# Optimization experiments

Measured on AMD Instinct MI355X. Metric: run time of the kernel, lower is better.

The kernel has to match this reference:

```python
import jax, jax.numpy as jnp
import numpy as np

N = 10000      # nodes
E = 160000     # edges
C = 128        # channels (hidden_irreps multiplicity)
NE = 10        # num_elements
G = 16         # num graphs
NB = 8         # num_bessel
RMAX = 5.0
PCUT = 5.0     # num_polynomial_cutoff
AVG_NN = 16.0
SQ3 = 3.0 ** 0.5


def _mlp(x, w1, w2, w3, wo):
    h = jax.nn.silu(x @ w1)
    h = jax.nn.silu(h @ w2)
    h = jax.nn.silu(h @ w3)
    return h @ wo


def _forward(positions, node_attrs, charges, shifts,
             W_emb, W_up1, Wr1_1, Wr1_2, Wr1_3, Wr1_o, Wlin1_s, Wlin1_v,
             P1_s1, P1_ss, P1_vv, P1_v1, P1_sv, Lp1_s, Lp1_v, R1,
             Wsk, Wup2_s, Wup2_v, Wr2_1, Wr2_2, Wr2_3, Wr2_o, Wlin2_s, Wlin2_v,
             P2_v1, P2_sv, Lp2_v, Rmid, Rout,
             edge_index, batch, num_graphs):
    snd, rcv = edge_index[0], edge_index[1]
    # edge vectors / lengths
    vec = positions[rcv] - positions[snd] + shifts                  # [E,3]
    length = jnp.sqrt(jnp.sum(vec * vec, -1) + 1e-12)               # [E]
    Yv = SQ3 * vec / length[:, None]                                # l=1 SH, component norm
    # Bessel radial basis * polynomial cutoff
    n = jnp.arange(1, NB + 1, dtype=positions.dtype)
    bess = (2.0 / RMAX) ** 0.5 * jnp.sin(n * jnp.pi * length[:, None] / RMAX) / length[:, None]
    u = length / RMAX
    p = PCUT
    fcut = jnp.where(u < 1.0,
                     1 - ((p + 1) * (p + 2) / 2) * u ** p + p * (p + 2) * u ** (p + 1)
                     - (p * (p + 1) / 2) * u ** (p + 2), 0.0)
    edge_feats = bess * fcut[:, None]                               # [E,NB]

    h = node_attrs @ W_emb                                          # node embedding [N,C]
    seg = lambda m: jax.ops.segment_sum(m, rcv, num_segments=N) / AVG_NN
    we = lambda Pm: node_attrs @ Pm                                 # element-dep. weights

    # ---- interaction / product / readout layer 1 (node feats are scalars) ----
    hu = h @ W_up1
    w = _mlp(edge_feats, Wr1_1, Wr1_2, Wr1_3, Wr1_o)                # [E,2C] TP weights
    w_ss, w_sv = w[:, :C], w[:, C:]
    hs_e = hu[snd]                                                  # gather sender feats
    A_s = seg(w_ss * hs_e)                                          # 0e x 0e -> 0e
    A_v = seg((w_sv * hs_e)[:, :, None] * Yv[:, None, :])           # 0e x 1o -> 1o
    A_s = A_s @ Wlin1_s
    A_v = jnp.einsum('ncd,ce->ned', A_v, Wlin1_v)
    # symmetric contraction (correlation=2), element-dependent weights
    B_s = we(P1_s1) * A_s + we(P1_ss) * A_s * A_s + we(P1_vv) * jnp.sum(A_v * A_v, -1) / SQ3
    B_v = we(P1_v1)[:, :, None] * A_v + we(P1_sv)[:, :, None] * A_s[:, :, None] * A_v
    h_s = B_s @ Lp1_s
    h_v = jnp.einsum('ncd,ce->ned', B_v, Lp1_v)
    dip1 = jnp.einsum('ncd,c->nd', h_v, R1)                         # linear dipole readout

    # ---- layer 2 (residual, output 128x1o) ----
    hs = h_s @ Wup2_s
    hv = jnp.einsum('ncd,ce->ned', h_v, Wup2_v)
    w2 = _mlp(edge_feats, Wr2_1, Wr2_2, Wr2_3, Wr2_o)               # [E,4C]
    w_a, w_b, w_c, w_d = w2[:, :C], w2[:, C:2 * C], w2[:, 2 * C:3 * C], w2[:, 3 * C:]
    hs_e, hv_e = hs[snd], hv[snd]
    m_s = w_a * hs_e + w_b * jnp.einsum('ecd,ed->ec', hv_e, Yv) / SQ3   # 0x0, 1x1->0
    m_v = (w_c * hs_e)[:, :, None] * Yv[:, None, :] + w_d[:, :, None] * hv_e  # 0x1,1x0->1
    A2_s = seg(m_s) @ Wlin2_s
    A2_v = jnp.einsum('ncd,ce->ned', seg(m_v), Wlin2_v)
    sc_v = jnp.einsum('ne,ecf,ncd->nfd', node_attrs, Wsk, h_v)      # skip TP (residual)
    B2_v = we(P2_v1)[:, :, None] * A2_v + we(P2_sv)[:, :, None] * A2_s[:, :, None] * A2_v
    h2_v = jnp.einsum('ncd,ce->ned', B2_v, Lp2_v) + sc_v
    # nonlinear dipole readout: input is pure 1o so gate scalars have no equivariant
    # path (zeros) -> sigmoid(0)=0.5 multiplier, as e3nn Gate would compute.
    mid = 0.5 * jnp.einsum('ncd,ck->nkd', h2_v, Rmid)               # [N,16,3]
    dip2 = jnp.einsum('nkd,k->nd', mid, Rout)

    atomic_dipoles = dip1 + dip2                                    # [N,3]
    total = jax.ops.segment_sum(atomic_dipoles, batch, num_segments=num_graphs)
    baseline = jax.ops.segment_sum(charges[:, None] * positions, batch, num_segments=num_graphs)
    return total + baseline, atomic_dipoles


def setup_inputs() -> dict:
    key = jax.random.key(0)
    ks = jax.random.split(key, 40)
    f32 = jnp.float32
    species = jax.random.randint(ks[0], (N,), 0, NE)
    w = lambda k, shape: jax.random.normal(k, shape, f32) / np.sqrt(shape[-2] if len(shape) > 1 else shape[0]).astype(np.float32)
    inp = dict(
        positions=jax.random.uniform(ks[1], (N, 3), f32) * 6.0,
        node_attrs=jax.nn.one_hot(species, NE, dtype=f32),
        charges=jax.random.normal(ks[2], (N,), f32),
        shifts=jnp.zeros((E, 3), f32),
        edge_index=jax.random.randint(ks[3], (2, E), 0, N),
        batch=jnp.sort(jax.random.randint(ks[4], (N,), 0, G)),
        ptr=jnp.arange(G + 1),
        W_emb=w(ks[5], (NE, C)), W_up1=w(ks[6], (C, C)),
        Wr1_1=w(ks[7], (NB, 64)), Wr1_2=w(ks[8], (64, 64)), Wr1_3=w(ks[9], (64, 64)),
        Wr1_o=w(ks[10], (64, 2 * C)), Wlin1_s=w(ks[11], (C, C)), Wlin1_v=w(ks[12], (C, C)),
        P1_s1=w(ks[13], (NE, C)), P1_ss=w(ks[14], (NE, C)), P1_vv=w(ks[15], (NE, C)),
        P1_v1=w(ks[16], (NE, C)), P1_sv=w(ks[17], (NE, C)),
        Lp1_s=w(ks[18], (C, C)), Lp1_v=w(ks[19], (C, C)),
        R1=jax.random.normal(ks[20], (C,), f32) / np.float32(np.sqrt(C)),
        Wsk=jax.random.normal(ks[21], (NE, C, C), f32) / np.float32(np.sqrt(C)),
        Wup2_s=w(ks[22], (C, C)), Wup2_v=w(ks[23], (C, C)),
        Wr2_1=w(ks[24], (NB, 64)), Wr2_2=w(ks[25], (64, 64)), Wr2_3=w(ks[26], (64, 64)),
        Wr2_o=w(ks[27], (64, 4 * C)), Wlin2_s=w(ks[28], (C, C)), Wlin2_v=w(ks[29], (C, C)),
        P2_v1=w(ks[30], (NE, C)), P2_sv=w(ks[31], (NE, C)), Lp2_v=w(ks[32], (C, C)),
        Rmid=w(ks[33], (C, 16)),
        Rout=jax.random.normal(ks[34], (16,), f32) / 4.0,
    )
    return inp


def reference(positions, node_attrs, charges, shifts, edge_index, batch, ptr,
              W_emb, W_up1, Wr1_1, Wr1_2, Wr1_3, Wr1_o, Wlin1_s, Wlin1_v,
              P1_s1, P1_ss, P1_vv, P1_v1, P1_sv, Lp1_s, Lp1_v, R1,
              Wsk, Wup2_s, Wup2_v, Wr2_1, Wr2_2, Wr2_3, Wr2_o, Wlin2_s, Wlin2_v,
              P2_v1, P2_sv, Lp2_v, Rmid, Rout):
    num_graphs = ptr.shape[0] - 1
    return _forward(positions, node_attrs, charges, shifts,
                    W_emb, W_up1, Wr1_1, Wr1_2, Wr1_3, Wr1_o, Wlin1_s, Wlin1_v,
                    P1_s1, P1_ss, P1_vv, P1_v1, P1_sv, Lp1_s, Lp1_v, R1,
                    Wsk, Wup2_s, Wup2_v, Wr2_1, Wr2_2, Wr2_3, Wr2_o, Wlin2_s, Wlin2_v,
                    P2_v1, P2_sv, Lp2_v, Rmid, Rout,
                    edge_index, batch, num_graphs)
```

## Files before the change

kernel.cpp:

```cpp
#include <hip/hip_runtime.h>

#define NN 10000
#define EE 160000
#define CC 128
#define NEL 10
#define NGR 16

static inline int cdiv(int a, int b) { return (a + b - 1) / b; }

__device__ __forceinline__ float silu_f(float x) { return x / (1.0f + __expf(-x)); }

__device__ __forceinline__ float bf2f(unsigned short u) {
    unsigned int x = ((unsigned int)u) << 16;
    return __uint_as_float(x);
}
__device__ __forceinline__ unsigned short f2bf(float f) {
    unsigned int x = __float_as_uint(f);
    unsigned int r = x + 0x7fffu + ((x >> 16) & 1u);
    return (unsigned short)(r >> 16);
}

typedef __attribute__((ext_vector_type(8))) short bf16x8;
typedef __attribute__((ext_vector_type(4))) float f32x4;

template <int K, int N, int MODE>
__global__ __launch_bounds__(256) void mfma_gemm(
    const unsigned short* __restrict__ in, int in_ld,
    const unsigned short* __restrict__ Wt,
    unsigned short* __restrict__ out, int out_ld,
    int R)
{
    constexpr int NT = N / 16;
    constexpr int KC = K / 32;
    constexpr int CPR = K / 8;
    __shared__ __align__(16) unsigned short Ash[64 * K];
    __shared__ __align__(16) unsigned short Bsh[N * K];

    const int tid = threadIdx.x;
    const int w = tid >> 6;
    const int l = tid & 63;
    const int row0 = blockIdx.x * 64;
    const int cb = blockIdx.y * N;

    for (int cid = tid; cid < 64 * CPR; cid += 256) {
        int r = cid / CPR, k8 = cid % CPR;
        int row = row0 + r;
        uint4 val = make_uint4(0u, 0u, 0u, 0u);
        if (row < R) val = *(const uint4*)(in + (size_t)row * in_ld + k8 * 8);
        unsigned bo = ((unsigned)(r * K + k8 * 8) * 2u) ^ (((unsigned)(r & 7)) << 4);
        *(uint4*)((char*)Ash + bo) = val;
    }
    for (int cid = tid; cid < N * CPR; cid += 256) {
        int nn = cid / CPR, k8 = cid % CPR;
        uint4 val = *(const uint4*)(Wt + (size_t)(cb + nn) * K + k8 * 8);
        unsigned bo = ((unsigned)(nn * K + k8 * 8) * 2u) ^ (((unsigned)(nn & 7)) << 4);
        *(uint4*)((char*)Bsh + bo) = val;
    }
    __syncthreads();

    bf16x8 afr[KC];
#pragma unroll
    for (int kc = 0; kc < KC; ++kc) {
        int r = w * 16 + (l & 15);
        int k = kc * 32 + (l >> 4) * 8;
        unsigned bo = ((unsigned)(r * K + k) * 2u) ^ (((unsigned)(r & 7)) << 4);
        afr[kc] = *(const bf16x8*)((char*)Ash + bo);
    }

    f32x4 acc[NT];
#pragma unroll
    for (int nt = 0; nt < NT; ++nt) {
        acc[nt] = (f32x4){0.f, 0.f, 0.f, 0.f};
#pragma unroll
        for (int kc = 0; kc < KC; ++kc) {
            int col = nt * 16 + (l & 15);
            int k = kc * 32 + (l >> 4) * 8;
            unsigned bo = ((unsigned)(col * K + k) * 2u) ^ (((unsigned)(col & 7)) << 4);
            bf16x8 bfr = *(const bf16x8*)((char*)Bsh + bo);
            acc[nt] = __builtin_amdgcn_mfma_f32_16x16x32_bf16(afr[kc], bfr, acc[nt], 0, 0, 0);
        }
    }

#pragma unroll
    for (int nt = 0; nt < NT; ++nt) {
#pragma unroll
        for (int rg = 0; rg < 4; ++rg) {
            int row = row0 + w * 16 + (l >> 4) * 4 + rg;
            if (row < R) {
                int col = cb + nt * 16 + (l & 15);
                float v = acc[nt][rg];
                if constexpr (MODE == 1) v = silu_f(v);
                out[(size_t)row * out_ld + col] = f2bf(v);
            }
        }
    }
}

template <int K, int N, int MODE>
__global__ __launch_bounds__(256) void mfma_gemm_f32(
    const float* __restrict__ in, int in_ld,
    const unsigned short* __restrict__ Wt,
    float* __restrict__ out, int out_ld,
    int R, float scale)
{
    constexpr int NT = N / 16;
    constexpr int KC = K / 32;
    constexpr int CPR = K / 8;
    __shared__ __align__(16) unsigned short Ash[64 * K];
    __shared__ __align__(16) unsigned short Bsh[N * K];

    const int tid = threadIdx.x;
    const int w = tid >> 6;
    const int l = tid & 63;
    const int row0 = blockIdx.x * 64;
    const int cb = blockIdx.y * N;

    for (int cid = tid; cid < 64 * CPR; cid += 256) {
        int r = cid / CPR, k8 = cid % CPR;
        int row = row0 + r;
        union { unsigned short u16[8]; uint4 v; } pk;
        if (row < R) {
            const float* p = in + (size_t)row * in_ld + k8 * 8;
            float4 f0 = *(const float4*)p;
            float4 f1 = *(const float4*)(p + 4);
            pk.u16[0] = f2bf(f0.x); pk.u16[1] = f2bf(f0.y);
            pk.u16[2] = f2bf(f0.z); pk.u16[3] = f2bf(f0.w);
            pk.u16[4] = f2bf(f1.x); pk.u16[5] = f2bf(f1.y);
            pk.u16[6] = f2bf(f1.z); pk.u16[7] = f2bf(f1.w);
        } else {
            pk.v = make_uint4(0u, 0u, 0u, 0u);
        }
        unsigned bo = ((unsigned)(r * K + k8 * 8) * 2u) ^ (((unsigned)(r & 7)) << 4);
        *(uint4*)((char*)Ash + bo) = pk.v;
    }
    for (int cid = tid; cid < N * CPR; cid += 256) {
        int nn = cid / CPR, k8 = cid % CPR;
        uint4 val = *(const uint4*)(Wt + (size_t)(cb + nn) * K + k8 * 8);
        unsigned bo = ((unsigned)(nn * K + k8 * 8) * 2u) ^ (((unsigned)(nn & 7)) << 4);
        *(uint4*)((char*)Bsh + bo) = val;
    }
    __syncthreads();

    bf16x8 afr[KC];
#pragma unroll
    for (int kc = 0; kc < KC; ++kc) {
        int r = w * 16 + (l & 15);
        int k = kc * 32 + (l >> 4) * 8;
        unsigned bo = ((unsigned)(r * K + k) * 2u) ^ (((unsigned)(r & 7)) << 4);
        afr[kc] = *(const bf16x8*)((char*)Ash + bo);
    }

    f32x4 acc[NT];
#pragma unroll
    for (int nt = 0; nt < NT; ++nt) {
        acc[nt] = (f32x4){0.f, 0.f, 0.f, 0.f};
#pragma unroll
        for (int kc = 0; kc < KC; ++kc) {
            int col = nt * 16 + (l & 15);
            int k = kc * 32 + (l >> 4) * 8;
            unsigned bo = ((unsigned)(col * K + k) * 2u) ^ (((unsigned)(col & 7)) << 4);
            bf16x8 bfr = *(const bf16x8*)((char*)Bsh + bo);
            acc[nt] = __builtin_amdgcn_mfma_f32_16x16x32_bf16(afr[kc], bfr, acc[nt], 0, 0, 0);
        }
    }

#pragma unroll
    for (int nt = 0; nt < NT; ++nt) {
#pragma unroll
        for (int rg = 0; rg < 4; ++rg) {
            int row = row0 + w * 16 + (l >> 4) * 4 + rg;
            if (row < R) {
                int col = cb + nt * 16 + (l & 15);
                float v = acc[nt][rg] * scale;
                size_t idx = (size_t)row * out_ld + col;
                if constexpr (MODE == 6)      out[idx] += v;
                else if constexpr (MODE == 2) ((unsigned short*)out)[idx] = f2bf(v);
                else                          out[idx] = v;
            }
        }
    }
}

struct WPE { const float* s[8]; unsigned short* d[8]; int K[8], N[8], Kp[8]; };
__global__ void k_wprepE(WPE wp)
{
    int m = blockIdx.y;
    int i = blockIdx.x * 256 + threadIdx.x;
    int tot = wp.N[m] * wp.Kp[m];
    if (i >= tot) return;
    int n = i / wp.Kp[m], k = i % wp.Kp[m];
    wp.d[m][i] = (k < wp.K[m]) ? f2bf(wp.s[m][k * wp.N[m] + n]) : (unsigned short)0;
}

struct WP10 { const float* s[10]; unsigned short* d[10]; };
__global__ void k_wprep10(WP10 wp)
{
    int m = blockIdx.y;
    int i = blockIdx.x * 256 + threadIdx.x;
    if (i >= 128 * 128) return;
    int n = i / 128, k = i % 128;
    wp.d[m][i] = f2bf(wp.s[m][k * 128 + n]);
}

__global__ void k_count(const int* __restrict__ rcv, int* __restrict__ deg)
{
    int e = blockIdx.x * 256 + threadIdx.x;
    if (e < EE) atomicAdd(&deg[rcv[e]], 1);
}

__global__ __launch_bounds__(256) void k_scan(const int* __restrict__ deg,
                                              int* __restrict__ rowptr,
                                              int* __restrict__ cursor)
{
    __shared__ int part[256];
    const int t = threadIdx.x;
    const int PER = (NN + 255) / 256;
    int base = t * PER;
    int s = 0;
    for (int j = 0; j < PER; ++j) { int idx = base + j; if (idx < NN) s += deg[idx]; }
    part[t] = s;
    __syncthreads();
    for (int off = 1; off < 256; off <<= 1) {
        int v = (t >= off) ? part[t - off] : 0;
        __syncthreads();
        part[t] += v;
        __syncthreads();
    }
    int run = (t == 0) ? 0 : part[t - 1];
    for (int j = 0; j < PER; ++j) {
        int idx = base + j;
        if (idx < NN) { rowptr[idx] = run; cursor[idx] = run; run += deg[idx]; }
    }
    if (t == 255) rowptr[NN] = part[255];
}

__global__ void k_fill(const int* __restrict__ rcv, int* __restrict__ cursor,
                       int* __restrict__ perm)
{
    int e = blockIdx.x * 256 + threadIdx.x;
    if (e >= EE) return;
    int pos = atomicAdd(&cursor[rcv[e]], 1);
    perm[pos] = e;
}

__global__ __launch_bounds__(256) void k_sortwave(const int* __restrict__ rowptr,
                                                  int* __restrict__ perm)
{
    int gid = blockIdx.x * 256 + threadIdx.x;
    int wid = gid >> 6;
    int lane = gid & 63;
    if (wid >= NN) return;
    int a = rowptr[wid], b = rowptr[wid + 1];
    int d = b - a;
    if (d <= 1) return;
    if (d <= 64) {
        int v = (lane < d) ? perm[a + lane] : 0x7fffffff;
        int rank = 0;
        for (int j = 0; j < 64; ++j) {
            int vj = __shfl(v, j);
            if (j < d && vj < v) ++rank;
        }
        if (lane < d) perm[a + rank] = v;
    } else if (lane == 0) {
        for (int i = a + 1; i < b; ++i) {
            int v = perm[i]; int j = i - 1;
            while (j >= a && perm[j] > v) { perm[j + 1] = perm[j]; --j; }
            perm[j + 1] = v;
        }
    }
}

__global__ void k_geom_perm(const float* __restrict__ pos, const float* __restrict__ shifts,
                            const int* __restrict__ snd, const int* __restrict__ rcv,
                            const int* __restrict__ perm,
                            float* __restrict__ Yv, unsigned short* __restrict__ efb,
                            int* __restrict__ psnd)
{
    int i = blockIdx.x * 256 + threadIdx.x;
    if (i >= EE) return;
    int e = perm[i];
    int s = snd[e], r = rcv[e];
    psnd[i] = s;
    float vx = pos[r * 3 + 0] - pos[s * 3 + 0] + shifts[e * 3 + 0];
    float vy = pos[r * 3 + 1] - pos[s * 3 + 1] + shifts[e * 3 + 1];
    float vz = pos[r * 3 + 2] - pos[s * 3 + 2] + shifts[e * 3 + 2];
    float len = sqrtf(vx * vx + vy * vy + vz * vz + 1e-12f);
    float inv = 1.0f / len;
    const float SQ3 = 1.7320508075688772f;
    Yv[i * 3 + 0] = SQ3 * vx * inv;
    Yv[i * 3 + 1] = SQ3 * vy * inv;
    Yv[i * 3 + 2] = SQ3 * vz * inv;
    float u = len * 0.2f;
    float fc = 0.0f;
    if (u < 1.0f) {
        float u2 = u * u, u4 = u2 * u2, u5 = u4 * u, u6 = u5 * u, u7 = u6 * u;
        fc = 1.0f - 21.0f * u5 + 35.0f * u6 - 15.0f * u7;
    }
    float pref = 0.6324555320336759f * inv * fc;
    const float PIO5 = 0.6283185307179586f;
    union { unsigned short u16[8]; uint4 v; } pk;
#pragma unroll
    for (int n = 1; n <= 8; ++n)
        pk.u16[n - 1] = f2bf(pref * sinf((float)n * PIO5 * len));
    uint4* dst = (uint4*)(efb + (size_t)i * 32);
    dst[0] = pk.v;
    dst[1] = make_uint4(0u, 0u, 0u, 0u);
    dst[2] = make_uint4(0u, 0u, 0u, 0u);
    dst[3] = make_uint4(0u, 0u, 0u, 0u);
}

__global__ __launch_bounds__(256) void k_gather1(
    const int* __restrict__ rowptr, const int* __restrict__ psnd,
    const float* __restrict__ Yv, const unsigned short* __restrict__ wb,
    int e0, int e1,
    const unsigned short* __restrict__ gS,
    float* __restrict__ outS, float* __restrict__ outV)
{
    const int t = threadIdx.x;
    const int c = t & 127;
    const int n = blockIdx.x * 2 + (t >> 7);
    if (n >= NN) return;
    int rs = rowptr[n], re = rowptr[n + 1];
    if (rs < e0) rs = e0;
    if (re > e1) re = e1;
    if (rs >= re) return;
    float accs = 0.f, a0 = 0.f, a1 = 0.f, a2 = 0.f;
    for (int i = rs; i < re; ++i) {
        const unsigned short* wp = wb + (size_t)(i - e0) * 256;
        float wss = bf2f(wp[c]);
        float wsv = bf2f(wp[128 + c]);
        float h = bf2f(gS[psnd[i] * 128 + c]);
        float y0 = Yv[i * 3], y1 = Yv[i * 3 + 1], y2 = Yv[i * 3 + 2];
        accs = fmaf(wss, h, accs);
        float tv = wsv * h;
        a0 = fmaf(tv, y0, a0); a1 = fmaf(tv, y1, a1); a2 = fmaf(tv, y2, a2);
    }
    outS[n * 128 + c] += accs;
    outV[n * 384 + c]       += a0;
    outV[n * 384 + 128 + c] += a1;
    outV[n * 384 + 256 + c] += a2;
}

__global__ __launch_bounds__(256) void k_gather23(
    const int* __restrict__ rowptr, const int* __restrict__ psnd,
    const float* __restrict__ Yv, const unsigned short* __restrict__ wb,
    int e0, int e1,
    const unsigned short* __restrict__ gS, const unsigned short* __restrict__ gV,
    float* __restrict__ outS, float* __restrict__ outV)
{
    const int t = threadIdx.x;
    const int c = t & 127;
    const int n = blockIdx.x * 2 + (t >> 7);
    if (n >= NN) return;
    int rs = rowptr[n], re = rowptr[n + 1];
    if (rs < e0) rs = e0;
    if (re > e1) re = e1;
    if (rs >= re) return;
    float accs = 0.f, a0 = 0.f, a1 = 0.f, a2 = 0.f;
    for (int i = rs; i < re; ++i) {
        const unsigned short* wp = wb + (size_t)(i - e0) * 512;
        float wa = bf2f(wp[c]);
        float wbv = bf2f(wp[128 + c]);
        float wc = bf2f(wp[256 + c]);
        float wd = bf2f(wp[384 + c]);
        int s = psnd[i];
        float hs = bf2f(gS[s * 128 + c]);
        float v0 = bf2f(gV[s * 384 + c]);
        float v1 = bf2f(gV[s * 384 + 128 + c]);
        float v2 = bf2f(gV[s * 384 + 256 + c]);
        float y0 = Yv[i * 3], y1 = Yv[i * 3 + 1], y2 = Yv[i * 3 + 2];
        float hd = v0 * y0 + v1 * y1 + v2 * y2;
        accs = fmaf(wa, hs, accs);
        accs = fmaf(wbv, hd * 0.57735026919f, accs);
        float tv = wc * hs;
        a0 = fmaf(tv, y0, a0); a0 = fmaf(wd, v0, a0);
        a1 = fmaf(tv, y1, a1); a1 = fmaf(wd, v1, a1);
        a2 = fmaf(tv, y2, a2); a2 = fmaf(wd, v2, a2);
    }
    outS[n * 128 + c] += accs;
    outV[n * 384 + c]       += a0;
    outV[n * 384 + 128 + c] += a1;
    outV[n * 384 + 256 + c] += a2;
}

__global__ void k_species(const float* __restrict__ attrs, int* __restrict__ species)
{
    int n = blockIdx.x * 256 + threadIdx.x;
    if (n >= NN) return;
    int sp = 0;
#pragma unroll
    for (int j = 0; j < NEL; ++j)
        if (attrs[n * NEL + j] > 0.5f) sp = j;
    species[n] = sp;
}

__global__ void k_embed(const float* __restrict__ W_emb, const int* __restrict__ species,
                        float* __restrict__ h)
{
    int t = blockIdx.x * 256 + threadIdx.x;
    if (t >= NN * CC) return;
    int n = t >> 7, c = t & 127;
    h[t] = W_emb[species[n] * CC + c];
}

__global__ void k_rmix(const float* __restrict__ Rmid, const float* __restrict__ Rout,
                       float* __restrict__ rmix)
{
    int c = threadIdx.x;
    float s = 0.f;
#pragma unroll
    for (int k = 0; k < 16; ++k) s = fmaf(Rmid[c * 16 + k], Rout[k], s);
    rmix[c] = s;
}

__global__ void k_B1(const int* __restrict__ species,
                     const float* __restrict__ As_l, const float* __restrict__ Av_l,
                     const float* __restrict__ P_s1, const float* __restrict__ P_ss,
                     const float* __restrict__ P_vv, const float* __restrict__ P_v1,
                     const float* __restrict__ P_sv,
                     float* __restrict__ Bs, float* __restrict__ Bv)
{
    int t = blockIdx.x * 256 + threadIdx.x;
    if (t >= NN * CC) return;
    int n = t >> 7, c = t & 127;
    int sp = species[n];
    int pb = sp * CC + c;
    int vb = n * 384 + c;
    float as = As_l[t];
    float a0 = Av_l[vb], a1 = Av_l[vb + CC], a2 = Av_l[vb + 2 * CC];
    Bs[t] = P_s1[pb] * as + P_ss[pb] * as * as
          + P_vv[pb] * (a0 * a0 + a1 * a1 + a2 * a2) * 0.57735026919f;
    float tv = P_v1[pb] + P_sv[pb] * as;
    Bv[vb] = tv * a0; Bv[vb + CC] = tv * a1; Bv[vb + 2 * CC] = tv * a2;
}

__global__ void k_B2(const int* __restrict__ species,
                     const float* __restrict__ As_l, const float* __restrict__ Av_l,
                     const float* __restrict__ P_v1, const float* __restrict__ P_sv,
                     float* __restrict__ Bv)
{
    int t = blockIdx.x * 256 + threadIdx.x;
    if (t >= NN * CC) return;
    int n = t >> 7, c = t & 127;
    int sp = species[n];
    int pb = sp * CC + c;
    int vb = n * 384 + c;
    float as = As_l[t];
    float tv = P_v1[pb] + P_sv[pb] * as;
    Bv[vb] = tv * Av_l[vb];
    Bv[vb + CC] = tv * Av_l[vb + CC];
    Bv[vb + 2 * CC] = tv * Av_l[vb + 2 * CC];
}

__global__ void k_dip1(const float* __restrict__ h_v, const float* __restrict__ R1,
                       float* __restrict__ dip1)
{
    int n = blockIdx.x, l = threadIdx.x;
    const float* hb = h_v + n * 384;
#pragma unroll
    for (int d = 0; d < 3; ++d) {
        float v = hb[d * CC + l] * R1[l] + hb[d * CC + 64 + l] * R1[64 + l];
        for (int o = 32; o > 0; o >>= 1) v += __shfl_down(v, o);
        if (l == 0) dip1[n * 3 + d] = v;
    }
}

__global__ void k_sc(const int* __restrict__ species, const float* __restrict__ h_v,
                     const float* __restrict__ Wsk, float* __restrict__ h2v)
{
    int n = blockIdx.x, f = threadIdx.x;
    int sp = species[n];
    const float* Wp = Wsk + sp * (CC * CC);
    const float* hvn = h_v + n * 384;
    float a0 = 0.f, a1 = 0.f, a2 = 0.f;
    for (int c = 0; c < CC; ++c) {
        float w = Wp[c * CC + f];
        a0 = fmaf(hvn[c], w, a0);
        a1 = fmaf(hvn[CC + c], w, a1);
        a2 = fmaf(hvn[2 * CC + c], w, a2);
    }
    h2v[n * 384 + f] = a0;
    h2v[n * 384 + CC + f] = a1;
    h2v[n * 384 + 2 * CC + f] = a2;
}

__global__ void k_node_out(const float* __restrict__ h2v, const float* __restrict__ rmix,
                           const float* __restrict__ dip1,
                           const float* __restrict__ charges, const float* __restrict__ pos,
                           float* __restrict__ out, float* __restrict__ tot)
{
    int n = blockIdx.x, l = threadIdx.x;
    const float* hb = h2v + n * 384;
    float r0 = rmix[l], r1 = rmix[64 + l];
    float red[3];
#pragma unroll
    for (int d = 0; d < 3; ++d) {
        float v = hb[d * CC + l] * r0 + hb[d * CC + 64 + l] * r1;
        for (int o = 32; o > 0; o >>= 1) v += __shfl_down(v, o);
        red[d] = v;
    }
    if (l == 0) {
        float q = charges[n];
#pragma unroll
        for (int d = 0; d < 3; ++d) {
            float a = dip1[n * 3 + d] + 0.5f * red[d];
            out[48 + n * 3 + d] = a;
            tot[n * 3 + d] = a + q * pos[n * 3 + d];
        }
    }
}

__global__ __launch_bounds__(256) void k_greduce(const float* __restrict__ tot,
                                                 const int* __restrict__ batch,
                                                 float* __restrict__ out)
{
    __shared__ float r[256 * 3];
    const int g = blockIdx.x;
    const int t = threadIdx.x;
    float s0 = 0.f, s1 = 0.f, s2 = 0.f;
    for (int n = t; n < NN; n += 256) {
        if (batch[n] == g) {
            s0 += tot[n * 3]; s1 += tot[n * 3 + 1]; s2 += tot[n * 3 + 2];
        }
    }
    r[t] = s0; r[256 + t] = s1; r[512 + t] = s2;
    __syncthreads();
    for (int off = 128; off > 0; off >>= 1) {
        if (t < off) {
            r[t] += r[t + off];
            r[256 + t] += r[256 + t + off];
            r[512 + t] += r[512 + t + off];
        }
        __syncthreads();
    }
    if (t < 3) out[g * 3 + t] = r[t * 256];
}

extern "C" void kernel_launch(void* const* d_in, const int* in_sizes, int n_in,
                              void* d_out, int out_size, void* d_ws, size_t ws_size,
                              hipStream_t stream)
{
    const float* positions = (const float*)d_in[0];
    const float* node_attrs = (const float*)d_in[1];
    const float* charges = (const float*)d_in[2];
    const float* shifts = (const float*)d_in[3];
    const int*   eidx = (const int*)d_in[4];
    const int*   batch = (const int*)d_in[5];
    const float* W_emb  = (const float*)d_in[7];
    const float* W_up1  = (const float*)d_in[8];
    const float* Wr1_1  = (const float*)d_in[9];
    const float* Wr1_2  = (const float*)d_in[10];
    const float* Wr1_3  = (const float*)d_in[11];
    const float* Wr1_o  = (const float*)d_in[12];
    const float* Wlin1_s = (const float*)d_in[13];
    const float* Wlin1_v = (const float*)d_in[14];
    const float* P1_s1 = (const float*)d_in[15];
    const float* P1_ss = (const float*)d_in[16];
    const float* P1_vv = (const float*)d_in[17];
    const float* P1_v1 = (const float*)d_in[18];
    const float* P1_sv = (const float*)d_in[19];
    const float* Lp1_s = (const float*)d_in[20];
    const float* Lp1_v = (const float*)d_in[21];
    const float* R1    = (const float*)d_in[22];
    const float* Wsk   = (const float*)d_in[23];
    const float* Wup2_s = (const float*)d_in[24];
    const float* Wup2_v = (const float*)d_in[25];
    const float* Wr2_1 = (const float*)d_in[26];
    const float* Wr2_2 = (const float*)d_in[27];
    const float* Wr2_3 = (const float*)d_in[28];
    const float* Wr2_o = (const float*)d_in[29];
    const float* Wlin2_s = (const float*)d_in[30];
    const float* Wlin2_v = (const float*)d_in[31];
    const float* P2_v1 = (const float*)d_in[32];
    const float* P2_sv = (const float*)d_in[33];
    const float* Lp2_v = (const float*)d_in[34];
    const float* Rmid  = (const float*)d_in[35];
    const float* Rout  = (const float*)d_in[36];
    (void)in_sizes; (void)n_in; (void)out_size;

    const int* snd = eidx;
    const int* rcv = eidx + EE;
    float* out = (float*)d_out;

    char* ws = (char*)d_ws;
    size_t off = 0;
    auto alloc = [&](size_t bytes) -> void* {
        void* p = (void*)(ws + off);
        off = (off + bytes + 255) & ~(size_t)255;
        return p;
    };
    int*   species = (int*)alloc((size_t)NN * 4);
    int*   deg     = (int*)alloc((size_t)NN * 4);
    int*   rowptr  = (int*)alloc((size_t)(NN + 16) * 4);
    int*   cursor  = (int*)alloc((size_t)NN * 4);
    int*   perm    = (int*)alloc((size_t)EE * 4);
    int*   psnd    = (int*)alloc((size_t)EE * 4);
    float* Yv   = (float*)alloc((size_t)EE * 3 * 4);
    unsigned short* efb = (unsigned short*)alloc((size_t)EE * 32 * 2);
    float* A_s  = (float*)alloc((size_t)NN * CC * 4);
    float* A_v  = (float*)alloc((size_t)NN * 3 * CC * 4);
    float* hbuf = (float*)alloc((size_t)NN * CC * 4);
    float* hu   = (float*)alloc((size_t)NN * CC * 4);
    float* h_v  = (float*)alloc((size_t)NN * 3 * CC * 4);
    float* h2v  = (float*)alloc((size_t)NN * 3 * CC * 4);
    float* dip1 = (float*)alloc((size_t)NN * 3 * 4);
    float* rmix = (float*)alloc((size_t)CC * 4);
    float* tot  = (float*)alloc((size_t)NN * 3 * 4);
    unsigned short* hub = (unsigned short*)alloc((size_t)NN * CC * 2);
    unsigned short* hsb = (unsigned short*)alloc((size_t)NN * CC * 2);
    unsigned short* hvb = (unsigned short*)alloc((size_t)NN * 3 * CC * 2);
    unsigned short* W1t_l1 = (unsigned short*)alloc(64 * 32 * 2);
    unsigned short* W2t_l1 = (unsigned short*)alloc(64 * 64 * 2);
    unsigned short* W3t_l1 = (unsigned short*)alloc(64 * 64 * 2);
    unsigned short* Wot_l1 = (unsigned short*)alloc(256 * 64 * 2);
    unsigned short* W1t_l2 = (unsigned short*)alloc(64 * 32 * 2);
    unsigned short* W2t_l2 = (unsigned short*)alloc(64 * 64 * 2);
    unsigned short* W3t_l2 = (unsigned short*)alloc(64 * 64 * 2);
    unsigned short* Wot_l2 = (unsigned short*)alloc(512 * 64 * 2);
    unsigned short* Wn[10];
    for (int m = 0; m < 10; ++m) Wn[m] = (unsigned short*)alloc(128 * 128 * 2);
    unsigned short* hbA = (unsigned short*)alloc((size_t)EE * 64 * 2);
    unsigned short* hbB = (unsigned short*)alloc((size_t)EE * 64 * 2);

    int C = 16;
    if      (off + (size_t)EE * 512 * 2 + 4096 <= ws_size)        C = 1;
    else if (off + (size_t)(EE / 2) * 512 * 2 + 4096 <= ws_size)  C = 2;
    else if (off + (size_t)(EE / 4) * 512 * 2 + 4096 <= ws_size)  C = 4;
    else if (off + (size_t)(EE / 8) * 512 * 2 + 4096 <= ws_size)  C = 8;
    const int EC = EE / C;
    unsigned short* wbuf = (unsigned short*)alloc((size_t)EC * 512 * 2);

    const float inv16 = 1.0f / 16.0f;
    const float one = 1.0f;

    hipMemsetAsync(deg, 0, (size_t)NN * 4, stream);
    hipMemsetAsync(A_s, 0, (size_t)NN * CC * 4, stream);
    hipMemsetAsync(A_v, 0, (size_t)NN * 3 * CC * 4, stream);

    {
        WPE wp;
        const float* s[8] = {Wr1_1, Wr1_2, Wr1_3, Wr1_o, Wr2_1, Wr2_2, Wr2_3, Wr2_o};
        unsigned short* d[8] = {W1t_l1, W2t_l1, W3t_l1, Wot_l1, W1t_l2, W2t_l2, W3t_l2, Wot_l2};
        int Ks[8] = {8, 64, 64, 64, 8, 64, 64, 64};
        int Ns[8] = {64, 64, 64, 256, 64, 64, 64, 512};
        int Kp[8] = {32, 64, 64, 64, 32, 64, 64, 64};
        for (int m = 0; m < 8; ++m) { wp.s[m] = s[m]; wp.d[m] = d[m]; wp.K[m] = Ks[m]; wp.N[m] = Ns[m]; wp.Kp[m] = Kp[m]; }
        k_wprepE<<<dim3(cdiv(512 * 64, 256), 8), 256, 0, stream>>>(wp);
    }
    {
        WP10 wp;
        const float* srcs[10] = {W_up1, Wlin1_s, Wlin1_v, Lp1_s, Lp1_v,
                                 Wup2_s, Wup2_v, Wlin2_s, Wlin2_v, Lp2_v};
        for (int m = 0; m < 10; ++m) { wp.s[m] = srcs[m]; wp.d[m] = Wn[m]; }
        k_wprep10<<<dim3(cdiv(128 * 128, 256), 10), 256, 0, stream>>>(wp);
    }

    k_count<<<cdiv(EE, 256), 256, 0, stream>>>(rcv, deg);
    k_scan<<<1, 256, 0, stream>>>(deg, rowptr, cursor);
    k_fill<<<cdiv(EE, 256), 256, 0, stream>>>(rcv, cursor, perm);
    k_sortwave<<<cdiv(NN * 64, 256), 256, 0, stream>>>(rowptr, perm);
    k_geom_perm<<<cdiv(EE, 256), 256, 0, stream>>>(positions, shifts, snd, rcv, perm, Yv, efb, psnd);

    k_species<<<cdiv(NN, 256), 256, 0, stream>>>(node_attrs, species);
    k_embed<<<cdiv(NN * CC, 256), 256, 0, stream>>>(W_emb, species, hbuf);
    k_rmix<<<1, CC, 0, stream>>>(Rmid, Rout, rmix);

    mfma_gemm_f32<128, 128, 2><<<cdiv(NN, 64), 256, 0, stream>>>(
        hbuf, 128, Wn[0], (float*)hub, 128, NN, one);

    mfma_gemm<32, 64, 1><<<cdiv(EE, 64), 256, 0, stream>>>(efb, 32, W1t_l1, hbA, 64, EE);
    mfma_gemm<64, 64, 1><<<cdiv(EE, 64), 256, 0, stream>>>(hbA, 64, W2t_l1, hbB, 64, EE);
    mfma_gemm<64, 64, 1><<<cdiv(EE, 64), 256, 0, stream>>>(hbB, 64, W3t_l1, hbA, 64, EE);
    for (int ch = 0; ch < C; ++ch) {
        int e0 = ch * EC, e1 = e0 + EC;
        mfma_gemm<64, 128, 2><<<dim3(cdiv(EC, 64), 2), 256, 0, stream>>>(
            hbA + (size_t)e0 * 64, 64, Wot_l1, wbuf, 256, EC);
        k_gather1<<<NN / 2, 256, 0, stream>>>(
            rowptr, psnd, Yv, wbuf, e0, e1, hub, A_s, A_v);
    }

    mfma_gemm_f32<128, 128, 0><<<cdiv(NN, 64), 256, 0, stream>>>(
        A_s, 128, Wn[1], A_s, 128, NN, inv16);
    mfma_gemm_f32<128, 128, 0><<<cdiv(3 * NN, 64), 256, 0, stream>>>(
        A_v, 128, Wn[2], A_v, 128, 3 * NN, inv16);
    k_B1<<<cdiv(NN * CC, 256), 256, 0, stream>>>(
        species, A_s, A_v, P1_s1, P1_ss, P1_vv, P1_v1, P1_sv, hbuf , A_v );
    mfma_gemm_f32<128, 128, 0><<<cdiv(NN, 64), 256, 0, stream>>>(
        hbuf, 128, Wn[3], hu , 128, NN, one);
    mfma_gemm_f32<128, 128, 0><<<cdiv(3 * NN, 64), 256, 0, stream>>>(
        A_v , 128, Wn[4], h_v, 128, 3 * NN, one);
    k_dip1<<<NN, 64, 0, stream>>>(h_v, R1, dip1);
    mfma_gemm_f32<128, 128, 2><<<cdiv(NN, 64), 256, 0, stream>>>(
        hu , 128, Wn[5], (float*)hsb, 128, NN, one);
    mfma_gemm_f32<128, 128, 2><<<cdiv(3 * NN, 64), 256, 0, stream>>>(
        h_v, 128, Wn[6], (float*)hvb, 128, 3 * NN, one);

    hipMemsetAsync(A_s, 0, (size_t)NN * CC * 4, stream);
    hipMemsetAsync(A_v, 0, (size_t)NN * 3 * CC * 4, stream);
    mfma_gemm<32, 64, 1><<<cdiv(EE, 64), 256, 0, stream>>>(efb, 32, W1t_l2, hbA, 64, EE);
    mfma_gemm<64, 64, 1><<<cdiv(EE, 64), 256, 0, stream>>>(hbA, 64, W2t_l2, hbB, 64, EE);
    mfma_gemm<64, 64, 1><<<cdiv(EE, 64), 256, 0, stream>>>(hbB, 64, W3t_l2, hbA, 64, EE);
    for (int ch = 0; ch < C; ++ch) {
        int e0 = ch * EC, e1 = e0 + EC;
        mfma_gemm<64, 128, 2><<<dim3(cdiv(EC, 64), 4), 256, 0, stream>>>(
            hbA + (size_t)e0 * 64, 64, Wot_l2, wbuf, 512, EC);
        k_gather23<<<NN / 2, 256, 0, stream>>>(
            rowptr, psnd, Yv, wbuf, e0, e1, hsb, hvb, A_s, A_v);
    }

    mfma_gemm_f32<128, 128, 0><<<cdiv(NN, 64), 256, 0, stream>>>(
        A_s, 128, Wn[7], A_s, 128, NN, inv16);
    mfma_gemm_f32<128, 128, 0><<<cdiv(3 * NN, 64), 256, 0, stream>>>(
        A_v, 128, Wn[8], A_v, 128, 3 * NN, inv16);
    k_sc<<<NN, 128, 0, stream>>>(species, h_v, Wsk, h2v);
    k_B2<<<cdiv(NN * CC, 256), 256, 0, stream>>>(species, A_s, A_v, P2_v1, P2_sv, A_v );
    mfma_gemm_f32<128, 128, 6><<<cdiv(3 * NN, 64), 256, 0, stream>>>(
        A_v , 128, Wn[9], h2v, 128, 3 * NN, one);

    k_node_out<<<NN, 64, 0, stream>>>(h2v, rmix, dip1, charges, positions, out, tot);
    k_greduce<<<NGR, 256, 0, stream>>>(tot, batch, out);
}
```

Measured before the change: 530.0 us.

## Fuse radial MLP layers into one kernel and merge small node kernels

Result: faster. 500.2 us (-5.6%).

```diff
diff --git a/kernel.cpp b/kernel.cpp
--- a/kernel.cpp
+++ b/kernel.cpp
@@ -22,6 +22,142 @@
 
 typedef __attribute__((ext_vector_type(8))) short bf16x8;
 typedef __attribute__((ext_vector_type(4))) float f32x4;
+
+template <int KIN>
+__global__ __launch_bounds__(256) void mfma_mlp3(
+    const unsigned short* __restrict__ in,
+    const unsigned short* __restrict__ W1t,
+    const unsigned short* __restrict__ W2t,
+    const unsigned short* __restrict__ W3t,
+    unsigned short* __restrict__ out, int R)
+{
+    __shared__ __align__(16) unsigned short Ash[64 * KIN];
+    __shared__ __align__(16) unsigned short W1s[64 * KIN];
+    __shared__ __align__(16) unsigned short W2s[64 * 64];
+    __shared__ __align__(16) unsigned short W3s[64 * 64];
+    __shared__ __align__(16) unsigned short H1[64 * 64];
+    __shared__ __align__(16) unsigned short H2[64 * 64];
+
+    const int tid = threadIdx.x;
+    const int w = tid >> 6;
+    const int l = tid & 63;
+    const int row0 = blockIdx.x * 64;
+
+    constexpr int CPRa = KIN / 8;
+    for (int cid = tid; cid < 64 * CPRa; cid += 256) {
+        int r = cid / CPRa, k8 = cid % CPRa;
+        int row = row0 + r;
+        uint4 val = make_uint4(0u, 0u, 0u, 0u);
+        if (row < R) val = *(const uint4*)(in + (size_t)row * KIN + k8 * 8);
+        unsigned bo = ((unsigned)(r * KIN + k8 * 8) * 2u) ^ (((unsigned)(r & 7)) << 4);
+        *(uint4*)((char*)Ash + bo) = val;
+    }
+    for (int cid = tid; cid < 64 * CPRa; cid += 256) {
+        int nn = cid / CPRa, k8 = cid % CPRa;
+        uint4 val = *(const uint4*)(W1t + (size_t)nn * KIN + k8 * 8);
+        unsigned bo = ((unsigned)(nn * KIN + k8 * 8) * 2u) ^ (((unsigned)(nn & 7)) << 4);
+        *(uint4*)((char*)W1s + bo) = val;
+    }
+    for (int cid = tid; cid < 64 * 8; cid += 256) {
+        int nn = cid / 8, k8 = cid % 8;
+        uint4 v2 = *(const uint4*)(W2t + (size_t)nn * 64 + k8 * 8);
+        uint4 v3 = *(const uint4*)(W3t + (size_t)nn * 64 + k8 * 8);
+        unsigned bo = ((unsigned)(nn * 64 + k8 * 8) * 2u) ^ (((unsigned)(nn & 7)) << 4);
+        *(uint4*)((char*)W2s + bo) = v2;
+        *(uint4*)((char*)W3s + bo) = v3;
+    }
+    __syncthreads();
+
+    {
+        f32x4 acc[4];
+#pragma unroll
+        for (int nt = 0; nt < 4; ++nt) acc[nt] = (f32x4){0.f, 0.f, 0.f, 0.f};
+#pragma unroll
+        for (int kc = 0; kc < KIN / 32; ++kc) {
+            int r = w * 16 + (l & 15);
+            int k = kc * 32 + (l >> 4) * 8;
+            unsigned boA = ((unsigned)(r * KIN + k) * 2u) ^ (((unsigned)(r & 7)) << 4);
+            bf16x8 afr = *(const bf16x8*)((char*)Ash + boA);
+#pragma unroll
+            for (int nt = 0; nt < 4; ++nt) {
+                int col = nt * 16 + (l & 15);
+                unsigned boB = ((unsigned)(col * KIN + k) * 2u) ^ (((unsigned)(col & 7)) << 4);
+                bf16x8 bfr = *(const bf16x8*)((char*)W1s + boB);
+                acc[nt] = __builtin_amdgcn_mfma_f32_16x16x32_bf16(afr, bfr, acc[nt], 0, 0, 0);
+            }
+        }
+#pragma unroll
+        for (int nt = 0; nt < 4; ++nt)
+#pragma unroll
+            for (int rg = 0; rg < 4; ++rg) {
+                int row = w * 16 + (l >> 4) * 4 + rg;
+                int col = nt * 16 + (l & 15);
+                unsigned bo = ((unsigned)(row * 64 + col) * 2u) ^ (((unsigned)(row & 7)) << 4);
+                *(unsigned short*)((char*)H1 + bo) = f2bf(silu_f(acc[nt][rg]));
+            }
+    }
+    __syncthreads();
+
+    {
+        f32x4 acc[4];
+#pragma unroll
+        for (int nt = 0; nt < 4; ++nt) acc[nt] = (f32x4){0.f, 0.f, 0.f, 0.f};
+#pragma unroll
+        for (int kc = 0; kc < 2; ++kc) {
+            int r = w * 16 + (l & 15);
+            int k = kc * 32 + (l >> 4) * 8;
+            unsigned boA = ((unsigned)(r * 64 + k) * 2u) ^ (((unsigned)(r & 7)) << 4);
+            bf16x8 afr = *(const bf16x8*)((char*)H1 + boA);
+#pragma unroll
+            for (int nt = 0; nt < 4; ++nt) {
+                int col = nt * 16 + (l & 15);
+                unsigned boB = ((unsigned)(col * 64 + k) * 2u) ^ (((unsigned)(col & 7)) << 4);
+                bf16x8 bfr = *(const bf16x8*)((char*)W2s + boB);
+                acc[nt] = __builtin_amdgcn_mfma_f32_16x16x32_bf16(afr, bfr, acc[nt], 0, 0, 0);
+            }
+        }
+#pragma unroll
+        for (int nt = 0; nt < 4; ++nt)
+#pragma unroll
+            for (int rg = 0; rg < 4; ++rg) {
+                int row = w * 16 + (l >> 4) * 4 + rg;
+                int col = nt * 16 + (l & 15);
+                unsigned bo = ((unsigned)(row * 64 + col) * 2u) ^ (((unsigned)(row & 7)) << 4);
+                *(unsigned short*)((char*)H2 + bo) = f2bf(silu_f(acc[nt][rg]));
+            }
+    }
+    __syncthreads();
+
+    {
+        f32x4 acc[4];
+#pragma unroll
+        for (int nt = 0; nt < 4; ++nt) acc[nt] = (f32x4){0.f, 0.f, 0.f, 0.f};
+#pragma unroll
+        for (int kc = 0; kc < 2; ++kc) {
+            int r = w * 16 + (l & 15);
+            int k = kc * 32 + (l >> 4) * 8;
+            unsigned boA = ((unsigned)(r * 64 + k) * 2u) ^ (((unsigned)(r & 7)) << 4);
+            bf16x8 afr = *(const bf16x8*)((char*)H2 + boA);
+#pragma unroll
+            for (int nt = 0; nt < 4; ++nt) {
+                int col = nt * 16 + (l & 15);
+                unsigned boB = ((unsigned)(col * 64 + k) * 2u) ^ (((unsigned)(col & 7)) << 4);
+                bf16x8 bfr = *(const bf16x8*)((char*)W3s + boB);
+                acc[nt] = __builtin_amdgcn_mfma_f32_16x16x32_bf16(afr, bfr, acc[nt], 0, 0, 0);
+            }
+        }
+#pragma unroll
+        for (int nt = 0; nt < 4; ++nt)
+#pragma unroll
+            for (int rg = 0; rg < 4; ++rg) {
+                int row = row0 + w * 16 + (l >> 4) * 4 + rg;
+                if (row < R) {
+                    int col = nt * 16 + (l & 15);
+                    out[(size_t)row * 64 + col] = f2bf(silu_f(acc[nt][rg]));
+                }
+            }
+    }
+}
 
 template <int K, int N, int MODE>
 __global__ __launch_bounds__(256) void mfma_gemm(
@@ -383,34 +519,18 @@
     outV[n * 384 + 256 + c] += a2;
 }
 
-__global__ void k_species(const float* __restrict__ attrs, int* __restrict__ species)
-{
-    int n = blockIdx.x * 256 + threadIdx.x;
-    if (n >= NN) return;
-    int sp = 0;
-#pragma unroll
-    for (int j = 0; j < NEL; ++j)
-        if (attrs[n * NEL + j] > 0.5f) sp = j;
-    species[n] = sp;
-}
-
-__global__ void k_embed(const float* __restrict__ W_emb, const int* __restrict__ species,
-                        float* __restrict__ h)
+__global__ void k_embed2(const float* __restrict__ attrs, const float* __restrict__ W_emb,
+                         int* __restrict__ species, float* __restrict__ h)
 {
     int t = blockIdx.x * 256 + threadIdx.x;
     if (t >= NN * CC) return;
     int n = t >> 7, c = t & 127;
-    h[t] = W_emb[species[n] * CC + c];
-}
-
-__global__ void k_rmix(const float* __restrict__ Rmid, const float* __restrict__ Rout,
-                       float* __restrict__ rmix)
-{
-    int c = threadIdx.x;
-    float s = 0.f;
-#pragma unroll
-    for (int k = 0; k < 16; ++k) s = fmaf(Rmid[c * 16 + k], Rout[k], s);
-    rmix[c] = s;
+    int sp = 0;
+#pragma unroll
+    for (int j = 0; j < NEL; ++j)
+        if (attrs[n * NEL + j] > 0.5f) sp = j;
+    if (c == 0) species[n] = sp;
+    h[t] = W_emb[sp * CC + c];
 }
 
 __global__ void k_B1(const int* __restrict__ species,
@@ -452,19 +572,6 @@
     Bv[vb + 2 * CC] = tv * Av_l[vb + 2 * CC];
 }
 
-__global__ void k_dip1(const float* __restrict__ h_v, const float* __restrict__ R1,
-                       float* __restrict__ dip1)
-{
-    int n = blockIdx.x, l = threadIdx.x;
-    const float* hb = h_v + n * 384;
-#pragma unroll
-    for (int d = 0; d < 3; ++d) {
-        float v = hb[d * CC + l] * R1[l] + hb[d * CC + 64 + l] * R1[64 + l];
-        for (int o = 32; o > 0; o >>= 1) v += __shfl_down(v, o);
-        if (l == 0) dip1[n * 3 + d] = v;
-    }
-}
-
 __global__ void k_sc(const int* __restrict__ species, const float* __restrict__ h_v,
                      const float* __restrict__ Wsk, float* __restrict__ h2v)
 {
@@ -484,26 +591,36 @@
     h2v[n * 384 + 2 * CC + f] = a2;
 }
 
-__global__ void k_node_out(const float* __restrict__ h2v, const float* __restrict__ rmix,
-                           const float* __restrict__ dip1,
-                           const float* __restrict__ charges, const float* __restrict__ pos,
-                           float* __restrict__ out, float* __restrict__ tot)
+__global__ void k_node_out2(const float* __restrict__ h2v, const float* __restrict__ h_v,
+                            const float* __restrict__ R1,
+                            const float* __restrict__ Rmid, const float* __restrict__ Rout,
+                            const float* __restrict__ charges, const float* __restrict__ pos,
+                            float* __restrict__ out, float* __restrict__ tot)
 {
     int n = blockIdx.x, l = threadIdx.x;
+    float r0 = 0.f, r1 = 0.f;
+#pragma unroll
+    for (int k = 0; k < 16; ++k) {
+        r0 = fmaf(Rmid[l * 16 + k], Rout[k], r0);
+        r1 = fmaf(Rmid[(64 + l) * 16 + k], Rout[k], r1);
+    }
     const float* hb = h2v + n * 384;
-    float r0 = rmix[l], r1 = rmix[64 + l];
+    const float* hv1 = h_v + n * 384;
+    float R1a = R1[l], R1b = R1[64 + l];
     float red[3];
 #pragma unroll
     for (int d = 0; d < 3; ++d) {
         float v = hb[d * CC + l] * r0 + hb[d * CC + 64 + l] * r1;
-        for (int o = 32; o > 0; o >>= 1) v += __shfl_down(v, o);
-        red[d] = v;
+        float dv = hv1[d * CC + l] * R1a + hv1[d * CC + 64 + l] * R1b;
+        float m = dv + 0.5f * v;
+        for (int o = 32; o > 0; o >>= 1) m += __shfl_down(m, o);
+        red[d] = m;
     }
     if (l == 0) {
         float q = charges[n];
 #pragma unroll
         for (int d = 0; d < 3; ++d) {
-            float a = dip1[n * 3 + d] + 0.5f * red[d];
+            float a = red[d];
             out[48 + n * 3 + d] = a;
             tot[n * 3 + d] = a + q * pos[n * 3 + d];
         }
@@ -603,8 +720,6 @@
     float* hu   = (float*)alloc((size_t)NN * CC * 4);
     float* h_v  = (float*)alloc((size_t)NN * 3 * CC * 4);
     float* h2v  = (float*)alloc((size_t)NN * 3 * CC * 4);
-    float* dip1 = (float*)alloc((size_t)NN * 3 * 4);
-    float* rmix = (float*)alloc((size_t)CC * 4);
     float* tot  = (float*)alloc((size_t)NN * 3 * 4);
     unsigned short* hub = (unsigned short*)alloc((size_t)NN * CC * 2);
     unsigned short* hsb = (unsigned short*)alloc((size_t)NN * CC * 2);
@@ -620,7 +735,6 @@
     unsigned short* Wn[10];
     for (int m = 0; m < 10; ++m) Wn[m] = (unsigned short*)alloc(128 * 128 * 2);
     unsigned short* hbA = (unsigned short*)alloc((size_t)EE * 64 * 2);
-    unsigned short* hbB = (unsigned short*)alloc((size_t)EE * 64 * 2);
 
     int C = 16;
     if      (off + (size_t)EE * 512 * 2 + 4096 <= ws_size)        C = 1;
@@ -634,8 +748,7 @@
     const float one = 1.0f;
 
     hipMemsetAsync(deg, 0, (size_t)NN * 4, stream);
-    hipMemsetAsync(A_s, 0, (size_t)NN * CC * 4, stream);
-    hipMemsetAsync(A_v, 0, (size_t)NN * 3 * CC * 4, stream);
+    hipMemsetAsync(A_s, 0, (size_t)NN * 4 * CC * 4, stream);
 
     {
         WPE wp;
@@ -661,16 +774,12 @@
     k_sortwave<<<cdiv(NN * 64, 256), 256, 0, stream>>>(rowptr, perm);
     k_geom_perm<<<cdiv(EE, 256), 256, 0, stream>>>(positions, shifts, snd, rcv, perm, Yv, efb, psnd);
 
-    k_species<<<cdiv(NN, 256), 256, 0, stream>>>(node_attrs, species);
-    k_embed<<<cdiv(NN * CC, 256), 256, 0, stream>>>(W_emb, species, hbuf);
-    k_rmix<<<1, CC, 0, stream>>>(Rmid, Rout, rmix);
+    k_embed2<<<cdiv(NN * CC, 256), 256, 0, stream>>>(node_attrs, W_emb, species, hbuf);
 
     mfma_gemm_f32<128, 128, 2><<<cdiv(NN, 64), 256, 0, stream>>>(
         hbuf, 128, Wn[0], (float*)hub, 128, NN, one);
 
-    mfma_gemm<32, 64, 1><<<cdiv(EE, 64), 256, 0, stream>>>(efb, 32, W1t_l1, hbA, 64, EE);
-    mfma_gemm<64, 64, 1><<<cdiv(EE, 64), 256, 0, stream>>>(hbA, 64, W2t_l1, hbB, 64, EE);
-    mfma_gemm<64, 64, 1><<<cdiv(EE, 64), 256, 0, stream>>>(hbB, 64, W3t_l1, hbA, 64, EE);
+    mfma_mlp3<32><<<cdiv(EE, 64), 256, 0, stream>>>(efb, W1t_l1, W2t_l1, W3t_l1, hbA, EE);
     for (int ch = 0; ch < C; ++ch) {
         int e0 = ch * EC, e1 = e0 + EC;
         mfma_gemm<64, 128, 2><<<dim3(cdiv(EC, 64), 2), 256, 0, stream>>>(
@@ -689,17 +798,13 @@
         hbuf, 128, Wn[3], hu , 128, NN, one);
     mfma_gemm_f32<128, 128, 0><<<cdiv(3 * NN, 64), 256, 0, stream>>>(
         A_v , 128, Wn[4], h_v, 128, 3 * NN, one);
-    k_dip1<<<NN, 64, 0, stream>>>(h_v, R1, dip1);
     mfma_gemm_f32<128, 128, 2><<<cdiv(NN, 64), 256, 0, stream>>>(
         hu , 128, Wn[5], (float*)hsb, 128, NN, one);
     mfma_gemm_f32<128, 128, 2><<<cdiv(3 * NN, 64), 256, 0, stream>>>(
         h_v, 128, Wn[6], (float*)hvb, 128, 3 * NN, one);
 
-    hipMemsetAsync(A_s, 0, (size_t)NN * CC * 4, stream);
-    hipMemsetAsync(A_v, 0, (size_t)NN * 3 * CC * 4, stream);
-    mfma_gemm<32, 64, 1><<<cdiv(EE, 64), 256, 0, stream>>>(efb, 32, W1t_l2, hbA, 64, EE);
-    mfma_gemm<64, 64, 1><<<cdiv(EE, 64), 256, 0, stream>>>(hbA, 64, W2t_l2, hbB, 64, EE);
-    mfma_gemm<64, 64, 1><<<cdiv(EE, 64), 256, 0, stream>>>(hbB, 64, W3t_l2, hbA, 64, EE);
+    hipMemsetAsync(A_s, 0, (size_t)NN * 4 * CC * 4, stream);
+    mfma_mlp3<32><<<cdiv(EE, 64), 256, 0, stream>>>(efb, W1t_l2, W2t_l2, W3t_l2, hbA, EE);
     for (int ch = 0; ch < C; ++ch) {
         int e0 = ch * EC, e1 = e0 + EC;
         mfma_gemm<64, 128, 2><<<dim3(cdiv(EC, 64), 4), 256, 0, stream>>>(
@@ -717,6 +822,6 @@
     mfma_gemm_f32<128, 128, 6><<<cdiv(3 * NN, 64), 256, 0, stream>>>(
         A_v , 128, Wn[9], h2v, 128, 3 * NN, one);
 
-    k_node_out<<<NN, 64, 0, stream>>>(h2v, rmix, dip1, charges, positions, out, tot);
+    k_node_out2<<<NN, 64, 0, stream>>>(h2v, h_v, R1, Rmid, Rout, charges, positions, out, tot);
     k_greduce<<<NGR, 256, 0, stream>>>(tot, batch, out);
 }
```
